# Kernel tuning notes

Measured on AMD Instinct MI355X. Metric: run time of the kernel, lower is better.

Reference implementation:

```python
import jax, jax.numpy as jnp
import numpy as np

N, D, K, TLEN = 2048, 64, 4, 2
DENSITY = 0.01  # avg degree ~20


def setup_inputs() -> dict:
    key = jax.random.key(0)
    k1, k2, k3, k4, k5, k6, k7 = jax.random.split(key, 7)
    attributes = jax.random.normal(k1, (N, D), dtype=jnp.float32)
    # binary adjacency, no self loops
    eye = jnp.eye(N, dtype=jnp.float32)
    edges = (jax.random.uniform(k2, (N, N)) < DENSITY).astype(jnp.float32) * (1.0 - eye)
    # two-hop neighbors: structure of edges @ edges with diagonal removed (Actor.train)
    two_hop = ((edges @ edges) > 0).astype(jnp.float32) * (1.0 - eye)
    persona = jax.random.uniform(k3, (TLEN, N, K), dtype=jnp.float32)
    T = jax.random.uniform(k4, (K,), minval=0.5, maxval=2.0, dtype=jnp.float32)
    e = jax.random.uniform(k5, (K,), minval=0.1, maxval=1.0, dtype=jnp.float32)
    r = jax.random.uniform(k6, (K,), minval=0.1, maxval=0.9, dtype=jnp.float32)
    W = jax.random.uniform(k7, (K,), minval=0.1, maxval=1.0, dtype=jnp.float32)
    return {"attributes": attributes, "edges": edges, "two_hop": two_hop,
            "persona": persona, "T": T, "e": e, "r": r, "W": W, "times": 1}


def reference(attributes, edges, two_hop, persona, T, e, r, W, times):
    n = attributes.shape[0]
    offdiag = ~jnp.eye(n, dtype=bool)
    # adj_sim only uses the sparsity STRUCTURE of the adjacency argument
    edge_mask = edges > 0                       # one-hop structure
    two_hop_mask = (edges + two_hop) > 0        # union structure (two_hop_range)
    K_ = persona.shape[-1]
    p_t = persona[times]                        # [N, K]

    edges_prob = jnp.zeros((n, n), dtype=attributes.dtype)
    attr_prob = jnp.zeros_like(attributes)
    for i in range(K_):
        neighbar_feat = (edges @ attributes) * W[i]
        next_feat = r[i] * attributes + neighbar_feat * (1.0 - r[i])   # [N, D]
        feat_sigmoid = jax.nn.sigmoid(next_feat)
        # calcu_l2: row-wise L2 normalization
        Fn = next_feat / jnp.sqrt(jnp.sum(next_feat * next_feat, axis=1, keepdims=True))
        # adj_sim with dense features == masked Gram matrix
        S = Fn @ Fn.T                                                   # [N, N]
        # two-hop branch: exp(S/T)*e then tanh_func (tanh + remove diagonal)
        conn = jnp.where(two_hop_mask & offdiag,
                         jnp.tanh(jnp.exp(S / T[i]) * e[i]), 0.0)
        # one-hop connect branch
        one_conn = jnp.where(edge_mask & offdiag,
                             jnp.tanh(jnp.exp(S / T[i]) * e[i]), 0.0)
        # delete branch uses dissimilarity 1 - S on one-hop structure
        delete = jnp.where(edge_mask & offdiag,
                           jnp.tanh(jnp.exp((1.0 - S) / T[i]) * e[i]), 0.0)
        common = one_conn * delete
        # overwrite_exit: on one-hop (off-diag) entries replace conn by common
        exit_prob = jnp.where(edge_mask & offdiag, common, conn)
        # persona[times][:, i] * sparse mat broadcasts over the last dim (columns)
        edges_prob = edges_prob + exit_prob * p_t[:, i][None, :]
        attr_prob = attr_prob + feat_sigmoid * p_t[:, i][:, None]
    return edges_prob, attr_prob
```

## Files before the change

### kernel.cpp

```cpp
#include <hip/hip_runtime.h>
#include <math.h>

#define N 2048
#define D 64
#define KP 4

typedef unsigned int uint;
typedef unsigned short ushort;
typedef unsigned long long u64;
typedef __attribute__((ext_vector_type(8))) short bf16x8;
typedef __attribute__((ext_vector_type(4))) float f32x4;
typedef __attribute__((ext_vector_type(4))) uint uint4v;

__device__ __forceinline__ ushort f2bf(float f) {
  uint u = __builtin_bit_cast(uint, f);
  u += 0x7FFFu + ((u >> 16) & 1u);
  return (ushort)(u >> 16);
}

__device__ __forceinline__ float tanh_pade(float x) {
  float y = fminf(x, 4.0f);
  float y2 = y * y;
  float p = y * (945.0f + y2 * (105.0f + y2));
  float q = 945.0f + y2 * (420.0f + y2 * 15.0f);
  return p * __builtin_amdgcn_rcpf(q);
}


__global__ __launch_bounds__(256) void row_kernel(
    const float* __restrict__ attr, const float* __restrict__ edges,
    const float* __restrict__ two_hop, const float* __restrict__ persona,
    const int* __restrict__ timesP, const float* __restrict__ rp,
    const float* __restrict__ Wp, ushort* __restrict__ Fnb,
    u64* __restrict__ ME, u64* __restrict__ MT, float* __restrict__ out)
{
  __shared__ float part[4][64];

  int t = threadIdx.x;
  int w = t >> 6, l = t & 63;
  int row = blockIdx.x;

  const float4* erow4 = reinterpret_cast<const float4*>(edges + (size_t)row * N);
  const float4* trow4 = reinterpret_cast<const float4*>(two_hop + (size_t)row * N);

  u64 mw[2][4];
  #pragma unroll
  for (int cc = 0; cc < 2; ++cc) {
    int chunk = 2 * w + cc;
    float4 ev = erow4[chunk * 64 + l];
    float4 tv = trow4[chunk * 64 + l];
    int colb = chunk * 256 + 4 * l;
    float evs[4] = {ev.x, ev.y, ev.z, ev.w};
    float tvs[4] = {tv.x, tv.y, tv.z, tv.w};
    #pragma unroll
    for (int jj = 0; jj < 4; ++jj) {
      bool eb = evs[jj] != 0.0f;
      u64 meb = __ballot(eb);
      u64 mtb = __ballot((eb || tvs[jj] != 0.0f) && (colb + jj != row));
      mw[cc][jj] = meb;
      if (l == jj) {
        ME[(size_t)row * 32 + chunk * 4 + jj] = meb;
        MT[(size_t)row * 32 + chunk * 4 + jj] = mtb;
      }
    }
  }

  float acc = 0.0f;
  #pragma unroll
  for (int cc = 0; cc < 2; ++cc) {
    #pragma unroll
    for (int jj = 0; jj < 4; ++jj) {
      u64 word = mw[cc][jj];
      int base = (2 * w + cc) * 256 + jj;
      while (word) {
        int b = __builtin_ctzll(word);
        word &= word - 1;
        acc += attr[(size_t)(base + 4 * b) * D + l];
      }
    }
  }
  part[w][l] = acc;
  __syncthreads();
  float ea = part[0][l] + part[1][l] + part[2][l] + part[3][l];
  __syncthreads();

  float a = attr[(size_t)row * D + l];
  float ri = rp[w], Wi = Wp[w];
  float nf = ri * a + ea * Wi * (1.0f - ri);
  float ss = nf * nf;
  #pragma unroll
  for (int off = 32; off; off >>= 1) ss += __shfl_xor(ss, off);
  float inv = rsqrtf(ss);
  Fnb[((size_t)w * N + row) * D + l] = f2bf(nf * inv);

  int times = timesP[0];
  float p = persona[((size_t)times * N + row) * KP + w];
  float sig = 1.0f / (1.0f + __expf(-nf));
  part[w][l] = p * sig;
  __syncthreads();
  if (w == 0) {
    out[(size_t)N * N + (size_t)row * D + l] =
        part[0][l] + part[1][l] + part[2][l] + part[3][l];
  }
}

__device__ __forceinline__ bf16x8 frag_read(const ushort* buf, int prow, int dbyte) {
  int off = prow * 128 + (dbyte ^ ((prow & 7) << 4));
  return *(const bf16x8*)((const char*)buf + off);
}

__global__ __launch_bounds__(256, 4) void edge_kernel(
    const u64* __restrict__ ME, const u64* __restrict__ MT,
    const float* __restrict__ persona, const int* __restrict__ timesP,
    const float* __restrict__ Tp, const float* __restrict__ ep,
    const ushort* __restrict__ Fnb, float* __restrict__ out)
{
  __shared__ ushort Ab[64 * 64];
  __shared__ ushort Bb[64 * 64];
  __shared__ u64 meL[64][4], mtL[64][4];

  int t = threadIdx.x;
  int w = t >> 6, l = t & 63;
  int wr = w >> 1, wc = w & 1;
  int lr = l >> 4, lc = l & 15;
  int row0 = blockIdx.y * 64;
  int col0 = blockIdx.x * 64;
  int times = timesP[0];

  {
    int rr = t >> 2, jj = t & 3;
    int cb4 = (col0 >> 8) * 4;
    meL[rr][jj] = ME[(size_t)(row0 + rr) * 32 + cb4 + jj];
    mtL[rr][jj] = MT[(size_t)(row0 + rr) * 32 + cb4 + jj];
  }
  __syncthreads();

  uint mem = 0, mtm = 0;
  {
    int j = lc & 3;
    int s0 = ((col0 & 255) >> 2) + wc * 8 + (lc >> 2);
    #pragma unroll
    for (int mt_ = 0; mt_ < 2; ++mt_) {
      #pragma unroll
      for (int jr = 0; jr < 4; ++jr) {
        int rowl = wr * 32 + mt_ * 16 + lr * 4 + jr;
        u64 mew = meL[rowl][j], mtw = mtL[rowl][j];
        #pragma unroll
        for (int nt_ = 0; nt_ < 2; ++nt_) {
          int bp = s0 + nt_ * 4;
          int b = (mt_ * 2 + nt_) * 4 + jr;
          mem |= (uint)((mew >> bp) & 1ull) << b;
          mtm |= (uint)((mtw >> bp) & 1ull) << b;
        }
      }
    }
  }

  float pc[KP][2];
  #pragma unroll
  for (int i = 0; i < KP; ++i) {
    #pragma unroll
    for (int nt_ = 0; nt_ < 2; ++nt_) {
      int col = col0 + wc * 32 + nt_ * 16 + lc;
      pc[i][nt_] = persona[((size_t)times * N + col) * KP + i];
    }
  }

  f32x4 acc[2][2] = {};

  #pragma unroll
  for (int i = 0; i < KP; ++i) {
    __syncthreads();
    {
      int r = t >> 2, q = t & 3;
      uint sw = (uint)((r & 7) << 4);
      const char* srcA = (const char*)(Fnb + ((size_t)i * N + row0 + r) * D);
      uint4v a0 = *(const uint4v*)(srcA + q * 32);
      uint4v a1 = *(const uint4v*)(srcA + q * 32 + 16);
      char* dstA = (char*)Ab + r * 128;
      *(uint4v*)(dstA + ((q * 32) ^ sw)) = a0;
      *(uint4v*)(dstA + ((q * 32 + 16) ^ sw)) = a1;
      const char* srcB = (const char*)(Fnb + ((size_t)i * N + col0 + r) * D);
      uint4v b0 = *(const uint4v*)(srcB + q * 32);
      uint4v b1 = *(const uint4v*)(srcB + q * 32 + 16);
      char* dstB = (char*)Bb + r * 128;
      *(uint4v*)(dstB + ((q * 32) ^ sw)) = b0;
      *(uint4v*)(dstB + ((q * 32 + 16) ^ sw)) = b1;
    }
    __syncthreads();

    f32x4 S[2][2] = {};
    #pragma unroll
    for (int ks = 0; ks < 2; ++ks) {
      int dbyte = ks * 64 + lr * 16;
      bf16x8 a0 = frag_read(Ab, wr * 32 + lc, dbyte);
      bf16x8 a1 = frag_read(Ab, wr * 32 + 16 + lc, dbyte);
      bf16x8 b0 = frag_read(Bb, wc * 32 + lc, dbyte);
      bf16x8 b1 = frag_read(Bb, wc * 32 + 16 + lc, dbyte);
      S[0][0] = __builtin_amdgcn_mfma_f32_16x16x32_bf16(a0, b0, S[0][0], 0, 0, 0);
      S[0][1] = __builtin_amdgcn_mfma_f32_16x16x32_bf16(a0, b1, S[0][1], 0, 0, 0);
      S[1][0] = __builtin_amdgcn_mfma_f32_16x16x32_bf16(a1, b0, S[1][0], 0, 0, 0);
      S[1][1] = __builtin_amdgcn_mfma_f32_16x16x32_bf16(a1, b1, S[1][1], 0, 0, 0);
    }

    float invT = 1.0f / Tp[i];
    float ei = ep[i];
    float di = ei * __expf(invT);
    #pragma unroll
    for (int mt_ = 0; mt_ < 2; ++mt_) {
      #pragma unroll
      for (int nt_ = 0; nt_ < 2; ++nt_) {
        float pcv = pc[i][nt_];
        int bb = (mt_ * 2 + nt_) * 4;
        float E[4], t1[4];
        #pragma unroll
        for (int j = 0; j < 4; ++j) E[j] = __expf(S[mt_][nt_][j] * invT);
        #pragma unroll
        for (int j = 0; j < 4; ++j) t1[j] = tanh_pade(E[j] * ei);
        #pragma unroll
        for (int j = 0; j < 4; ++j) {
          if ((mem >> (bb + j)) & 1) {
            t1[j] *= tanh_pade(di * __builtin_amdgcn_rcpf(E[j]));
          }
        }
        #pragma unroll
        for (int j = 0; j < 4; ++j) {
          acc[mt_][nt_][j] += ((mtm >> (bb + j)) & 1) ? t1[j] * pcv : 0.0f;
        }
      }
    }
  }

  #pragma unroll
  for (int mt_ = 0; mt_ < 2; ++mt_) {
    #pragma unroll
    for (int nt_ = 0; nt_ < 2; ++nt_) {
      #pragma unroll
      for (int j = 0; j < 4; ++j) {
        int row = row0 + wr * 32 + mt_ * 16 + lr * 4 + j;
        int col = col0 + wc * 32 + nt_ * 16 + lc;
        out[(size_t)row * N + col] = acc[mt_][nt_][j];
      }
    }
  }
}

extern "C" void kernel_launch(void* const* d_in, const int* in_sizes, int n_in,
                              void* d_out, int out_size, void* d_ws, size_t ws_size,
                              hipStream_t stream) {
  const float* attributes = (const float*)d_in[0];
  const float* edges      = (const float*)d_in[1];
  const float* two_hop    = (const float*)d_in[2];
  const float* persona    = (const float*)d_in[3];
  const float* Tp         = (const float*)d_in[4];
  const float* ep         = (const float*)d_in[5];
  const float* rp         = (const float*)d_in[6];
  const float* Wp         = (const float*)d_in[7];
  const int*   timesP     = (const int*)d_in[8];
  float* out = (float*)d_out;

  ushort* Fnb = (ushort*)d_ws;
  u64* ME = (u64*)((char*)d_ws + (size_t)KP * N * D * 2);
  u64* MT = ME + (size_t)N * 32;

  row_kernel<<<N, 256, 0, stream>>>(attributes, edges, two_hop, persona,
                                    timesP, rp, Wp, Fnb, ME, MT, out);
  edge_kernel<<<dim3(N / 64, N / 64), 256, 0, stream>>>(
      ME, MT, persona, timesP, Tp, ep, Fnb, out);
}
```

Measured before the change: 34.28 us.

## Replace exp/tanh chain with Chebyshev polynomial fit of similarity transfer

Block 0 of the row kernel now fits degree-11 Chebyshev polynomials to the per-persona functions tanh(e·exp(S/T)) and its product with the delete term over S in [-1.03, 1.03]. It converts them to monomial coefficients in workspace. The edge kernel then evaluates these polynomials with Horner FMAs instead of calling exp, rcp and Pade tanh per element. This trades transcendental work for about 11-22 FMAs per element, and the result is accurate only to the fit error. Since S is a cosine similarity bounded in [-1,1], the approximation holds for any valid input.

After: 35.73 us. +4.2%, slower.

```diff
diff --git a/kernel.cpp b/kernel.cpp
--- a/kernel.cpp
+++ b/kernel.cpp
@@ -4,6 +4,9 @@
 #define N 2048
 #define D 64
 #define KP 4
+#define PI_F 3.14159265358979f
+#define ADOM 1.03f
+#define NDEG 12
 
 typedef unsigned int uint;
 typedef unsigned short ushort;
@@ -12,27 +15,36 @@
 typedef __attribute__((ext_vector_type(4))) float f32x4;
 typedef __attribute__((ext_vector_type(4))) uint uint4v;
 
+__device__ static const float TCmat[12][12] = {
+  {   1,   0,    0,    0,    0,     0,    0,     0,     0,     0,    0,    0},
+  {   0,   1,    0,    0,    0,     0,    0,     0,     0,     0,    0,    0},
+  {  -1,   0,    2,    0,    0,     0,    0,     0,     0,     0,    0,    0},
+  {   0,  -3,    0,    4,    0,     0,    0,     0,     0,     0,    0,    0},
+  {   1,   0,   -8,    0,    8,     0,    0,     0,     0,     0,    0,    0},
+  {   0,   5,    0,  -20,    0,    16,    0,     0,     0,     0,    0,    0},
+  {  -1,   0,   18,    0,  -48,     0,   32,     0,     0,     0,    0,    0},
+  {   0,  -7,    0,   56,    0,  -112,    0,    64,     0,     0,    0,    0},
+  {   1,   0,  -32,    0,  160,     0, -256,     0,   128,     0,    0,    0},
+  {   0,   9,    0, -120,    0,   432,    0,  -576,     0,   256,    0,    0},
+  {  -1,   0,   50,    0, -400,     0, 1120,     0, -1280,     0,  512,    0},
+  {   0, -11,    0,  220,    0, -1232,    0,  2816,     0, -2816,    0, 1024},
+};
+
 __device__ __forceinline__ ushort f2bf(float f) {
   uint u = __builtin_bit_cast(uint, f);
   u += 0x7FFFu + ((u >> 16) & 1u);
   return (ushort)(u >> 16);
 }
 
-__device__ __forceinline__ float tanh_pade(float x) {
-  float y = fminf(x, 4.0f);
-  float y2 = y * y;
-  float p = y * (945.0f + y2 * (105.0f + y2));
-  float q = 945.0f + y2 * (420.0f + y2 * 15.0f);
-  return p * __builtin_amdgcn_rcpf(q);
-}
-
 
 __global__ __launch_bounds__(256) void row_kernel(
     const float* __restrict__ attr, const float* __restrict__ edges,
     const float* __restrict__ two_hop, const float* __restrict__ persona,
     const int* __restrict__ timesP, const float* __restrict__ rp,
-    const float* __restrict__ Wp, ushort* __restrict__ Fnb,
-    u64* __restrict__ ME, u64* __restrict__ MT, float* __restrict__ out)
+    const float* __restrict__ Wp, const float* __restrict__ Tp,
+    const float* __restrict__ ep, ushort* __restrict__ Fnb,
+    u64* __restrict__ ME, u64* __restrict__ MT, float* __restrict__ coefs,
+    float* __restrict__ out)
 {
   __shared__ float part[4][64];
 
@@ -102,6 +114,42 @@
     out[(size_t)N * N + (size_t)row * D + l] =
         part[0][l] + part[1][l] + part[2][l] + part[3][l];
   }
+
+  if (row == 0) {
+    __syncthreads();
+    float invT = 1.0f / Tp[w];
+    float ei = ep[w];
+    int k = l & 31;
+    float x = cosf(PI_F * (k + 0.5f) / 32.0f);
+    float s = ADOM * x;
+    float fv = tanhf(ei * expf(s * invT));
+    float hv = fv * tanhf(ei * expf((1.0f - s) * invT));
+    part[w][l] = (l < 32) ? fv : hv;
+    __syncthreads();
+    int j = l & 15;
+    bool doF = (l < 12);
+    bool doH = (l >= 16 && l < 28);
+    float c = 0.0f;
+    if (doF || doH) {
+      const float* vv = doF ? &part[w][0] : &part[w][32];
+      for (int kk = 0; kk < 32; ++kk) {
+        c += vv[kk] * cosf(PI_F * j * (kk + 0.5f) / 32.0f);
+      }
+      c *= (j == 0) ? (1.0f / 32.0f) : (2.0f / 32.0f);
+    }
+    __syncthreads();
+    if (doF) part[w][j] = c;
+    if (doH) part[w][32 + j] = c;
+    __syncthreads();
+    if (doF || doH) {
+      const float* cc = doF ? &part[w][0] : &part[w][32];
+      float m = 0.0f;
+      #pragma unroll
+      for (int jj = 0; jj < 12; ++jj) m += cc[jj] * TCmat[jj][j];
+      m *= powf(1.0f / ADOM, (float)j);
+      coefs[w * 2 * NDEG + (doF ? 0 : NDEG) + j] = m;
+    }
+  }
 }
 
 __device__ __forceinline__ bf16x8 frag_read(const ushort* buf, int prow, int dbyte) {
@@ -112,8 +160,8 @@
 __global__ __launch_bounds__(256, 4) void edge_kernel(
     const u64* __restrict__ ME, const u64* __restrict__ MT,
     const float* __restrict__ persona, const int* __restrict__ timesP,
-    const float* __restrict__ Tp, const float* __restrict__ ep,
-    const ushort* __restrict__ Fnb, float* __restrict__ out)
+    const float* __restrict__ coefs, const ushort* __restrict__ Fnb,
+    float* __restrict__ out)
 {
   __shared__ ushort Ab[64 * 64];
   __shared__ ushort Bb[64 * 64];
@@ -203,29 +251,31 @@
       S[1][1] = __builtin_amdgcn_mfma_f32_16x16x32_bf16(a1, b1, S[1][1], 0, 0, 0);
     }
 
-    float invT = 1.0f / Tp[i];
-    float ei = ep[i];
-    float di = ei * __expf(invT);
+    float cF[NDEG], cH[NDEG];
+    #pragma unroll
+    for (int jj = 0; jj < NDEG; ++jj) {
+      cF[jj] = coefs[i * 2 * NDEG + jj];
+      cH[jj] = coefs[i * 2 * NDEG + NDEG + jj];
+    }
     #pragma unroll
     for (int mt_ = 0; mt_ < 2; ++mt_) {
       #pragma unroll
       for (int nt_ = 0; nt_ < 2; ++nt_) {
         float pcv = pc[i][nt_];
         int bb = (mt_ * 2 + nt_) * 4;
-        float E[4], t1[4];
-        #pragma unroll
-        for (int j = 0; j < 4; ++j) E[j] = __expf(S[mt_][nt_][j] * invT);
-        #pragma unroll
-        for (int j = 0; j < 4; ++j) t1[j] = tanh_pade(E[j] * ei);
         #pragma unroll
         for (int j = 0; j < 4; ++j) {
+          float sv = fminf(fmaxf(S[mt_][nt_][j], -ADOM), ADOM);
+          float v = cF[NDEG - 1];
+          #pragma unroll
+          for (int jj = NDEG - 2; jj >= 0; --jj) v = fmaf(v, sv, cF[jj]);
           if ((mem >> (bb + j)) & 1) {
-            t1[j] *= tanh_pade(di * __builtin_amdgcn_rcpf(E[j]));
+            float vh = cH[NDEG - 1];
+            #pragma unroll
+            for (int jj = NDEG - 2; jj >= 0; --jj) vh = fmaf(vh, sv, cH[jj]);
+            v = vh;
           }
-        }
-        #pragma unroll
-        for (int j = 0; j < 4; ++j) {
-          acc[mt_][nt_][j] += ((mtm >> (bb + j)) & 1) ? t1[j] * pcv : 0.0f;
+          acc[mt_][nt_][j] += ((mtm >> (bb + j)) & 1) ? v * pcv : 0.0f;
         }
       }
     }
@@ -262,9 +312,11 @@
   ushort* Fnb = (ushort*)d_ws;
   u64* ME = (u64*)((char*)d_ws + (size_t)KP * N * D * 2);
   u64* MT = ME + (size_t)N * 32;
+  float* coefs = (float*)(MT + (size_t)N * 32);
 
   row_kernel<<<N, 256, 0, stream>>>(attributes, edges, two_hop, persona,
-                                    timesP, rp, Wp, Fnb, ME, MT, out);
+                                    timesP, rp, Wp, Tp, ep, Fnb, ME, MT,
+                                    coefs, out);
   edge_kernel<<<dim3(N / 64, N / 64), 256, 0, stream>>>(
-      ME, MT, persona, timesP, Tp, ep, Fnb, out);
-}
+      ME, MT, persona, timesP, coefs, Fnb, out);
+}
```
